# Kernel optimization log

Hardware: AMD Instinct MI355X
Metric: run time of the kernel (lower is better)

## Reference

```python
import jax, jax.numpy as jnp
import numpy as np

D = 256      # d_model
SUB = 3      # number of adjacency subsets
GROUPS = 8
N, T, V = 32, 256, 19


def setup_inputs() -> dict:
    key = jax.random.key(0)
    ks = jax.random.split(key, 4)
    return {
        "x": jax.random.normal(ks[0], (N, T, V, D), jnp.float32),
        "para": jax.random.normal(ks[1], (3, GROUPS, V, V), jnp.float32),
        "linear_weight": jax.random.normal(ks[2], (D, D * SUB), jnp.float32) * 0.05,
        "linear_bias": jax.random.normal(ks[3], (1, D * SUB, 1, 1), jnp.float32) * 0.05,
        "bn_gamma": jnp.ones((D * SUB,), jnp.float32),
        "bn_beta": jnp.zeros((D * SUB,), jnp.float32),
        "bn1_gamma": jnp.ones((D,), jnp.float32),
        "bn1_beta": jnp.zeros((D,), jnp.float32),
    }


def _bn(x, gamma, beta, eps=1e-5):
    # BatchNorm2d (training mode): stats over (n, t, v) per channel
    m = jnp.mean(x, axis=(0, 2, 3), keepdims=True)
    v = jnp.var(x, axis=(0, 2, 3), keepdims=True)
    return (x - m) * jax.lax.rsqrt(v + eps) * gamma[None, :, None, None] + beta[None, :, None, None]


def reference(x, para, linear_weight, linear_bias, bn_gamma, bn_beta, bn1_gamma, bn1_beta):
    xc = jnp.transpose(x, (0, 3, 1, 2))                 # (n, c, t, v)
    # expand per-group adjacency to per-channel: (3, D, V, V)
    A = jnp.tile(para, (1, D // GROUPS, 1, 1))
    # L2 row-normalize along last dim (matches torch.norm(dim=-1))
    A = A / (jnp.linalg.norm(A, axis=-1, keepdims=True) + 1e-4)
    # channel mixing: (n, 3c, t, v)
    y = jnp.einsum('nctw,cd->ndtw', xc, linear_weight)
    y = _bn(y + linear_bias, bn_gamma, bn_beta)
    n, kc, t, v = y.shape
    y = y.reshape(n, SUB, kc // SUB, t, v)              # (n, k, c, t, v)
    # per-channel tiny 19x19 adjacency matmul
    y = jnp.einsum('nkctv,kcvw->nctw', y, A)            # (n, c, t, v)
    out = jax.nn.relu(_bn(y + xc, bn1_gamma, bn1_beta))
    return jnp.transpose(out, (0, 2, 3, 1))             # (n, t, v, c)
```

## Files before the change

### kernel.cpp

```cpp
#include <hip/hip_runtime.h>

typedef unsigned short u16;
typedef unsigned int u32;
typedef float f32x4 __attribute__((ext_vector_type(4)));
typedef __bf16 bf16x8 __attribute__((ext_vector_type(8)));

#define M_ALL 155648.0f
#define GP 168

__device__ __forceinline__ u16 f2bf(float f) {
  union { float f; u32 u; } x; x.f = f;
  u32 u = x.u;
  u += 0x7FFFu + ((u >> 16) & 1u);
  return (u16)(u >> 16);
}
__device__ __forceinline__ float bf2f(u16 h) {
  union { u32 u; float f; } x; x.u = ((u32)h) << 16;
  return x.f;
}
__device__ __forceinline__ f32x4 zero4() { f32x4 z = {0.f, 0.f, 0.f, 0.f}; return z; }

__device__ __forceinline__ int xs_idx(int m, int c) {
  return m * 256 + ((((c >> 3) ^ (m & 7)) << 3) | (c & 7));
}
__device__ __forceinline__ int y2_idx(int r, int kvp) {
  int sw = (r & 7) ^ ((r >> 3) & 7);
  return r * 64 + ((((kvp >> 3) ^ sw) << 3) | (kvp & 7));
}

__global__ void k_prep(const float* __restrict__ para, u16* __restrict__ wa2) {
  __shared__ float aL[3 * 8 * 19 * 19];
  int tid = threadIdx.x;
  if (tid < 456) {
    int k = tid / 152, rem = tid % 152, g = rem / 19, v = rem % 19;
    int base = ((k * 8 + g) * 19 + v) * 19;
    float ss = 0.f;
    #pragma unroll
    for (int w = 0; w < 19; ++w) { float a = para[base + w]; ss += a * a; }
    float inv = 1.f / (sqrtf(ss) + 1e-4f);
    #pragma unroll
    for (int w = 0; w < 19; ++w) aL[base + w] = para[base + w] * inv;
  }
  __syncthreads();
  for (int i = tid; i < 8 * 20 * 64; i += 512) {
    int g = i / 1280, rem = i % 1280, w = rem >> 6, kvp = rem & 63;
    u16 val = 0;
    if (w < 19 && kvp < 57) {
      int k = kvp / 19, v = kvp - 19 * k;
      val = f2bf(aL[((k * 8 + g) * 19 + v) * 19 + w]);
    }
    wa2[i] = val;
  }
}

__global__ void k_wt(const float* __restrict__ W, u16* __restrict__ wt) {
  int idx = blockIdx.x * 512 + threadIdx.x;
  int d = idx >> 8, c = idx & 255;
  wt[idx] = f2bf(W[c * 768 + d]);
}

__global__ __launch_bounds__(512, 2) void k_gram(const float* __restrict__ x,
                                                 float* __restrict__ G,
                                                 float* __restrict__ colsum) {
  __shared__ u16 xsT[256 * GP];
  __shared__ float scs[512];
  int tid = threadIdx.x, bid = blockIdx.x;
  int c = tid & 255, mh = tid >> 8;
  int lane = tid & 63, wave = tid >> 6;
  int cl = lane & 15, q = lane >> 4;

  if (tid < 256) {
    *reinterpret_cast<uint2*>(&xsT[tid * GP + 152]) = make_uint2(0u, 0u);
    *reinterpret_cast<uint2*>(&xsT[tid * GP + 156]) = make_uint2(0u, 0u);
  }

  float cs = 0.f;
  f32x4 acc[2][16];
  #pragma unroll
  for (int ri = 0; ri < 2; ++ri)
    #pragma unroll
    for (int j = 0; j < 16; ++j) acc[ri][j] = zero4();

  for (int ss = 0; ss < 4; ++ss) {
    int sl = bid * 4 + ss;
    const float* xb = x + (size_t)sl * 152 * 256;
    __syncthreads();
    #pragma unroll 1
    for (int it = 0; it < 19; ++it) {
      int m0 = it * 8 + mh * 4;
      float v0 = xb[(m0 + 0) * 256 + c];
      float v1 = xb[(m0 + 1) * 256 + c];
      float v2 = xb[(m0 + 2) * 256 + c];
      float v3 = xb[(m0 + 3) * 256 + c];
      cs += v0 + v1 + v2 + v3;
      uint2 p;
      p.x = (u32)f2bf(v0) | ((u32)f2bf(v1) << 16);
      p.y = (u32)f2bf(v2) | ((u32)f2bf(v3) << 16);
      *reinterpret_cast<uint2*>(&xsT[c * GP + m0]) = p;
    }
    __syncthreads();
    #pragma unroll
    for (int s = 0; s < 5; ++s) {
      int kof = s * 32 + q * 8;
      bf16x8 a0 = *reinterpret_cast<const bf16x8*>(&xsT[(wave * 16 + cl) * GP + kof]);
      bf16x8 a1 = *reinterpret_cast<const bf16x8*>(&xsT[((wave + 8) * 16 + cl) * GP + kof]);
      #pragma unroll
      for (int ct2 = 0; ct2 < 16; ++ct2) {
        bf16x8 b = *reinterpret_cast<const bf16x8*>(&xsT[(ct2 * 16 + cl) * GP + kof]);
        acc[0][ct2] = __builtin_amdgcn_mfma_f32_16x16x32_bf16(a0, b, acc[0][ct2], 0, 0, 0);
        acc[1][ct2] = __builtin_amdgcn_mfma_f32_16x16x32_bf16(a1, b, acc[1][ct2], 0, 0, 0);
      }
    }
  }
  #pragma unroll
  for (int ri = 0; ri < 2; ++ri) {
    int ct = wave + ri * 8;
    #pragma unroll
    for (int ct2 = 0; ct2 < 16; ++ct2) {
      if (ct2 >= ct) {
        #pragma unroll
        for (int r4 = 0; r4 < 4; ++r4)
          atomicAdd(&G[(ct * 16 + q * 4 + r4) * 256 + ct2 * 16 + cl], acc[ri][ct2][r4]);
      }
    }
  }
  scs[tid] = cs;
  __syncthreads();
  if (tid < 256) atomicAdd(&colsum[tid], scs[tid] + scs[tid + 256]);
}

__global__ void k_sym(float* __restrict__ G) {
  int i = blockIdx.x * 256 + threadIdx.x;
  int r = i >> 8, cN = i & 255;
  if (r > cN) G[i] = G[cN * 256 + r];
}

__global__ __launch_bounds__(256) void k_f1(const float* __restrict__ G,
                                            const float* __restrict__ colsum,
                                            const float* __restrict__ W,
                                            const float* __restrict__ gam,
                                            const float* __restrict__ bet,
                                            float* __restrict__ ST) {
  __shared__ float wd[256];
  __shared__ float red[16];
  int d = blockIdx.x, c = threadIdx.x;
  float wv = W[c * 768 + d];
  wd[c] = wv;
  __syncthreads();
  float dot = 0.f;
  const float* Gr = G + c * 256;
  #pragma unroll 4
  for (int j = 0; j < 256; ++j) dot += Gr[j] * wd[j];
  float part = wv * dot;
  float mpart = colsum[c] * wv;
  #pragma unroll
  for (int o = 32; o; o >>= 1) { part += __shfl_down(part, o); mpart += __shfl_down(mpart, o); }
  int lane = c & 63, w = c >> 6;
  if (lane == 0) { red[w] = part; red[8 + w] = mpart; }
  __syncthreads();
  if (c == 0) {
    float qv = red[0] + red[1] + red[2] + red[3];
    float ms = red[8] + red[9] + red[10] + red[11];
    float mean = ms / M_ALL;
    float var = qv / M_ALL - mean * mean;
    float S = gam[d] * rsqrtf(var + 1e-5f);
    ST[d] = S;
    ST[768 + d] = bet[d] - mean * S;
  }
}

__global__ __launch_bounds__(512, 2) void k_main(const float* __restrict__ x,
                                                 const u16* __restrict__ wt,
                                                 const u16* __restrict__ wa2,
                                                 const float* __restrict__ ST,
                                                 float* __restrict__ sumz,
                                                 float* __restrict__ out) {
  __shared__ u16 xs[152 * 256];
  __shared__ u16 y2[512 * 64];
  __shared__ float scrz[1024];
  int tid = threadIdx.x;
  int bid = blockIdx.x;
  const float* xbase = x + (size_t)bid * 152 * 256;
  size_t obase = (size_t)bid * 152 * 256;

  {
    int r = tid >> 6, c4 = (tid & 63) << 2;
    for (int it = 0; it < 19; ++it) {
      int m = it * 8 + r;
      float4 f = *reinterpret_cast<const float4*>(xbase + m * 256 + c4);
      uint2 p;
      p.x = (u32)f2bf(f.x) | ((u32)f2bf(f.y) << 16);
      p.y = (u32)f2bf(f.z) | ((u32)f2bf(f.w) << 16);
      *reinterpret_cast<uint2*>(&xs[xs_idx(m, c4)]) = p;
    }
  }

  int lane = tid & 63, wave = tid >> 6;
  int mhalf = wave & 1, nt3 = wave >> 1;
  int cl = lane & 15, q = lane >> 4;
  int g = wave;
  const bf16x8* wtv = reinterpret_cast<const bf16x8*>(wt);
  float* zbufF = reinterpret_cast<float*>(y2);

  bf16x8 bfr[2][2];
  #pragma unroll
  for (int ks = 0; ks < 2; ++ks)
    #pragma unroll
    for (int nt = 0; nt < 2; ++nt) {
      int w = nt * 16 + cl; int wc = (w < 20) ? w : 19;
      bfr[ks][nt] = *reinterpret_cast<const bf16x8*>(&wa2[(g * 20 + wc) * 64 + ks * 32 + q * 8]);
    }

  int arow[5], mlow[5];
  #pragma unroll
  for (int i = 0; i < 5; ++i) {
    int rr = mhalf * 80 + i * 16 + cl;
    if (rr > 151) rr = 151;
    arow[i] = rr * 256; mlow[i] = rr & 7;
  }
  __syncthreads();

  for (int nc = 0; nc < 4; ++nc) {
    f32x4 acc[5][3];
    #pragma unroll
    for (int i = 0; i < 5; ++i)
      #pragma unroll
      for (int jj = 0; jj < 3; ++jj) acc[i][jj] = zero4();
    for (int s = 0; s < 8; ++s) {
      int sq4 = s * 4 + q;
      bf16x8 b[3];
      #pragma unroll
      for (int jj = 0; jj < 3; ++jj) {
        int j = nt3 * 3 + jj;
        int d = (j >> 2) * 256 + nc * 64 + (j & 3) * 16 + cl;
        b[jj] = wtv[d * 32 + sq4];
      }
      #pragma unroll
      for (int i = 0; i < 5; ++i) {
        bf16x8 a = *reinterpret_cast<const bf16x8*>(&xs[arow[i] + ((sq4 ^ mlow[i]) << 3)]);
        #pragma unroll
        for (int jj = 0; jj < 3; ++jj)
          acc[i][jj] = __builtin_amdgcn_mfma_f32_16x16x32_bf16(a, b[jj], acc[i][jj], 0, 0, 0);
      }
    }
    __syncthreads();

    #pragma unroll
    for (int kk = 0; kk < 7; ++kk)
      y2[y2_idx(tid, 57 + kk)] = 0;

    #pragma unroll
    for (int jj = 0; jj < 3; ++jj) {
      int j = nt3 * 3 + jj;
      int ksub = j >> 2;
      int c_local = (j & 3) * 16 + cl;
      int d = ksub * 256 + nc * 64 + c_local;
      float Sc = ST[d], Tc = ST[768 + d];
      #pragma unroll
      for (int i = 0; i < 5; ++i) {
        int mb = mhalf * 80 + i * 16 + q * 4;
        #pragma unroll
        for (int r4 = 0; r4 < 4; ++r4) {
          int m = mb + r4;
          if (m < 152) {
            int t = (m * 27) >> 9;
            int v = m - t * 19;
            int kvp = ksub * 19 + v;
            int r = t * 64 + c_local;
            y2[y2_idx(r, kvp)] = f2bf(acc[i][jj][r4] * Sc + Tc);
          }
        }
      }
    }
    __syncthreads();

    f32x4 zacc[4][2];
    #pragma unroll
    for (int mt = 0; mt < 4; ++mt) { zacc[mt][0] = zero4(); zacc[mt][1] = zero4(); }
    #pragma unroll
    for (int ks = 0; ks < 2; ++ks) {
      #pragma unroll
      for (int mt = 0; mt < 4; ++mt) {
        int tc = mt * 16 + cl;
        int t = tc >> 3, c8 = tc & 7;
        int r = t * 64 + c8 * 8 + g;
        int ch = (ks * 4 + q) ^ g ^ c8;
        bf16x8 afr = *reinterpret_cast<const bf16x8*>(&y2[r * 64 + (ch << 3)]);
        #pragma unroll
        for (int nt = 0; nt < 2; ++nt)
          zacc[mt][nt] = __builtin_amdgcn_mfma_f32_16x16x32_bf16(afr, bfr[ks][nt], zacc[mt][nt], 0, 0, 0);
      }
    }
    __syncthreads();

    #pragma unroll
    for (int mt = 0; mt < 4; ++mt)
      #pragma unroll
      for (int nt = 0; nt < 2; ++nt) {
        int w = nt * 16 + cl;
        if (w < 19) {
          #pragma unroll
          for (int r4 = 0; r4 < 4; ++r4) {
            int mm = mt * 16 + q * 4 + r4;
            int t = mm >> 3, c8 = mm & 7;
            zbufF[(c8 * 8 + g) * 153 + t * 19 + w] = zacc[mt][nt][r4];
          }
        }
      }
    __syncthreads();

    float sz = 0.f, sq = 0.f;
    int cloc = tid & 63;
    int cglob = nc * 64 + cloc;
    #pragma unroll 1
    for (int rep = 0; rep < 19; ++rep) {
      int mp = rep * 8 + (tid >> 6);
      float z = zbufF[cloc * 153 + mp] + bf2f(xs[xs_idx(mp, cglob)]);
      out[obase + (size_t)mp * 256 + cglob] = z;
      sz += z; sq += z * z;
    }
    scrz[(tid >> 6) * 64 + cloc] = sz;
    scrz[512 + (tid >> 6) * 64 + cloc] = sq;
    __syncthreads();
    if (tid < 128) {
      int comp = tid >> 6, c = tid & 63;
      float v = 0.f;
      #pragma unroll
      for (int h = 0; h < 8; ++h) v += scrz[comp * 512 + h * 64 + c];
      atomicAdd(&sumz[comp * 256 + nc * 64 + c], v);
    }
  }
}

__global__ void k_f2(const float* __restrict__ statz, const float* __restrict__ gam,
                     const float* __restrict__ bet, float* __restrict__ S1T1) {
  int c = threadIdx.x;
  float inv = 1.f / M_ALL;
  float mz = statz[c] * inv;
  float qv = statz[256 + c] * inv;
  float var = qv - mz * mz;
  float Sc = gam[c] * rsqrtf(var + 1e-5f);
  S1T1[c] = Sc;
  S1T1[256 + c] = bet[c] - mz * Sc;
}

__global__ __launch_bounds__(256) void k_relu(float* __restrict__ out,
                                              const float* __restrict__ S1T1) {
  int tid = threadIdx.x;
  int lane = tid & 63;
  int wv = ((blockIdx.x << 8) + tid) >> 6;
  const float4* s14 = reinterpret_cast<const float4*>(S1T1);
  float4 sv = s14[lane], tv = s14[64 + lane];
  float4* o4 = reinterpret_cast<float4*>(out);
  #pragma unroll 1
  for (int r = 0; r < 19; ++r) {
    size_t i = ((size_t)r * 8192 + wv) * 64 + lane;
    float4 f = o4[i];
    f.x = fmaxf(f.x * sv.x + tv.x, 0.f);
    f.y = fmaxf(f.y * sv.y + tv.y, 0.f);
    f.z = fmaxf(f.z * sv.z + tv.z, 0.f);
    f.w = fmaxf(f.w * sv.w + tv.w, 0.f);
    o4[i] = f;
  }
}

extern "C" void kernel_launch(void* const* d_in, const int* in_sizes, int n_in,
                              void* d_out, int out_size, void* d_ws, size_t ws_size,
                              hipStream_t stream) {
  const float* x    = (const float*)d_in[0];
  const float* para = (const float*)d_in[1];
  const float* W    = (const float*)d_in[2];
  const float* bng  = (const float*)d_in[4];
  const float* bnb  = (const float*)d_in[5];
  const float* bn1g = (const float*)d_in[6];
  const float* bn1b = (const float*)d_in[7];
  float* out = (float*)d_out;

  char* ws = (char*)d_ws;
  u16* wt     = (u16*)ws;
  u16* wa2    = (u16*)(ws + 393216);
  float* G    = (float*)(ws + 413696);
  float* csum = (float*)(ws + 675840);
  float* sumz = (float*)(ws + 676864);
  float* ST   = (float*)(ws + 678912);
  float* S1T1 = (float*)(ws + 685056);

  hipMemsetAsync(ws + 413696, 0, 262144 + 1024 + 2048, stream);
  k_prep<<<dim3(1),    dim3(512), 0, stream>>>(para, wa2);
  k_wt  <<<dim3(384),  dim3(512), 0, stream>>>(W, wt);
  k_gram<<<dim3(256),  dim3(512), 0, stream>>>(x, G, csum);
  k_sym <<<dim3(256),  dim3(256), 0, stream>>>(G);
  k_f1  <<<dim3(768),  dim3(256), 0, stream>>>(G, csum, W, bng, bnb, ST);
  k_main<<<dim3(1024), dim3(512), 0, stream>>>(x, wt, wa2, ST, sumz, out);
  k_f2  <<<dim3(1),    dim3(256), 0, stream>>>(sumz, bn1g, bn1b, S1T1);
  k_relu<<<dim3(2048), dim3(256), 0, stream>>>(out, S1T1);
}
```

Measured before the change: 631.7 us.

## Replace Gram atomics with per-block partial tiles and a deterministic reduce kernel

Each k_gram block now writes its upper-triangular 16x16 Gram tiles to a private partial buffer with plain stores instead of doing atomicAdd into a shared G. A new k_red kernel sums the 256 block partials for each of the 136 tile pairs and writes both the tile and its mirror into G. This replaces the k_sym pass and shrinks the memset. The aim is to remove contention from 256 blocks atomically adding into the same addresses, at the cost of about 35 MB of extra partial-buffer write and read traffic.

New measurement: 608.2 us. 3.7% less time.

```diff
diff --git a/kernel.cpp b/kernel.cpp
--- a/kernel.cpp
+++ b/kernel.cpp
@@ -60,7 +60,7 @@
 }
 
 __global__ __launch_bounds__(512, 2) void k_gram(const float* __restrict__ x,
-                                                 float* __restrict__ G,
+                                                 float* __restrict__ Gp,
                                                  float* __restrict__ colsum) {
   __shared__ u16 xsT[256 * GP];
   __shared__ float scs[512];
@@ -115,12 +115,14 @@
   #pragma unroll
   for (int ri = 0; ri < 2; ++ri) {
     int ct = wave + ri * 8;
+    int tb = 16 * ct - (ct * (ct - 1)) / 2 - ct;
     #pragma unroll
     for (int ct2 = 0; ct2 < 16; ++ct2) {
       if (ct2 >= ct) {
+        float* dst = Gp + ((size_t)(tb + ct2) * 256 + bid) * 256;
         #pragma unroll
         for (int r4 = 0; r4 < 4; ++r4)
-          atomicAdd(&G[(ct * 16 + q * 4 + r4) * 256 + ct2 * 16 + cl], acc[ri][ct2][r4]);
+          dst[(q * 4 + r4) * 16 + cl] = acc[ri][ct2][r4];
       }
     }
   }
@@ -129,10 +131,23 @@
   if (tid < 256) atomicAdd(&colsum[tid], scs[tid] + scs[tid + 256]);
 }
 
-__global__ void k_sym(float* __restrict__ G) {
-  int i = blockIdx.x * 256 + threadIdx.x;
-  int r = i >> 8, cN = i & 255;
-  if (r > cN) G[i] = G[cN * 256 + r];
+__global__ __launch_bounds__(256) void k_red(const float* __restrict__ Gp,
+                                             float* __restrict__ G) {
+  int b = blockIdx.x;
+  int e = threadIdx.x;
+  int ct = 0;
+  #pragma unroll
+  for (int t = 1; t < 16; ++t)
+    if (b >= 16 * t - (t * (t - 1)) / 2) ct = t;
+  int ct2 = ct + (b - (16 * ct - (ct * (ct - 1)) / 2));
+  const float* src = Gp + (size_t)b * 65536;
+  float s = 0.f;
+  #pragma unroll 8
+  for (int p = 0; p < 256; ++p) s += src[p * 256 + e];
+  int row = e >> 4, col = e & 15;
+  int rr = ct * 16 + row, cc = ct2 * 16 + col;
+  G[rr * 256 + cc] = s;
+  G[cc * 256 + rr] = s;
 }
 
 __global__ __launch_bounds__(256) void k_f1(const float* __restrict__ G,
@@ -384,12 +399,13 @@
   float* sumz = (float*)(ws + 676864);
   float* ST   = (float*)(ws + 678912);
   float* S1T1 = (float*)(ws + 685056);
-
-  hipMemsetAsync(ws + 413696, 0, 262144 + 1024 + 2048, stream);
+  float* Gp   = (float*)(ws + 687104);
+
+  hipMemsetAsync(ws + 675840, 0, 1024 + 2048, stream);
   k_prep<<<dim3(1),    dim3(512), 0, stream>>>(para, wa2);
   k_wt  <<<dim3(384),  dim3(512), 0, stream>>>(W, wt);
-  k_gram<<<dim3(256),  dim3(512), 0, stream>>>(x, G, csum);
-  k_sym <<<dim3(256),  dim3(256), 0, stream>>>(G);
+  k_gram<<<dim3(256),  dim3(512), 0, stream>>>(x, Gp, csum);
+  k_red <<<dim3(136),  dim3(256), 0, stream>>>(Gp, G);
   k_f1  <<<dim3(768),  dim3(256), 0, stream>>>(G, csum, W, bng, bnb, ST);
   k_main<<<dim3(1024), dim3(512), 0, stream>>>(x, wt, wa2, ST, sumz, out);
   k_f2  <<<dim3(1),    dim3(256), 0, stream>>>(sumz, bn1g, bn1b, S1T1);
```
